# Performance work log

Measured on AMD Instinct MI355X. Metric: run time of the kernel, lower is better.

Reference implementation:

```python
import jax, jax.numpy as jnp
import numpy as np

B, S, H, NH = 2, 2048, 1024, 16
HD = H // NH  # head dim = 64


def setup_inputs() -> dict:
    key = jax.random.key(0)
    ks = jax.random.split(key, 11)
    s = 1.0 / np.sqrt(H)
    return {
        "q": jax.random.normal(ks[0], (B, S, H), jnp.float32),
        "k": jax.random.normal(ks[1], (B, S, H), jnp.float32),
        "v": jax.random.normal(ks[2], (B, S, H), jnp.float32),
        "Wq": jax.random.normal(ks[3], (H, H), jnp.float32) * s,
        "bq": jax.random.normal(ks[4], (H,), jnp.float32) * 0.02,
        "Wk": jax.random.normal(ks[5], (H, H), jnp.float32) * s,
        "bk": jax.random.normal(ks[6], (H,), jnp.float32) * 0.02,
        "Wv": jax.random.normal(ks[7], (H, H), jnp.float32) * s,
        "bv": jax.random.normal(ks[8], (H,), jnp.float32) * 0.02,
        "Wo": jax.random.normal(ks[9], (H, H), jnp.float32) * s,
        "bo": jax.random.normal(ks[10], (H,), jnp.float32) * 0.02,
    }


def reference(q, k, v, Wq, bq, Wk, bk, Wv, bv, Wo, bo):
    # QKV projections: [B,S,H]
    qp = q @ Wq + bq
    kp = k @ Wk + bk
    vp = v @ Wv + bv
    # split heads -> [B, NH, S, HD]
    def split(x):
        return x.reshape(B, S, NH, HD).transpose(0, 2, 1, 3)
    qh, kh, vh = split(qp), split(kp), split(vp)
    # scores [B, NH, S, S], scale by sqrt(head_dim)
    scores = jnp.einsum('bhqd,bhkd->bhqk', qh, kh) / jnp.sqrt(jnp.asarray(HD, qh.dtype))
    attn = jax.nn.softmax(scores, axis=-1)  # attention_dropout p=0.0 (eval)
    ctx = jnp.einsum('bhqk,bhkd->bhqd', attn, vh)
    # merge heads -> [B, S, H]
    ctx = ctx.transpose(0, 2, 1, 3).reshape(B, S, H)
    out = ctx @ Wo + bo  # dropout p=0.0 (eval)
    return out
```

## Files before the change

### kernel.cpp

```cpp
#include <hip/hip_runtime.h>

typedef unsigned short u16;
typedef __attribute__((ext_vector_type(8))) short bf16x8;
typedef __attribute__((ext_vector_type(4))) float f32x4;
typedef __attribute__((ext_vector_type(16))) float f32x16;
typedef __attribute__((ext_vector_type(4))) unsigned short u16x4;
typedef __attribute__((ext_vector_type(4))) unsigned int u32x4;

#define B_  2
#define S_  2048
#define H_  1024
#define NH_ 16
#define HD_ 64
#define MR_ (B_*S_)
#define K_  H_

__device__ __forceinline__ u16 f2bf(float f) {
  union { float f; unsigned u; } x; x.f = f;
  unsigned r = x.u + 0x7fffu + ((x.u >> 16) & 1u);
  return (u16)(r >> 16);
}

__device__ __forceinline__ unsigned cvtpk(float lo, float hi) {
  unsigned r;
  asm("v_cvt_pk_bf16_f32 %0, %1, %2" : "=v"(r) : "v"(lo), "v"(hi));
  return r;
}

__device__ __forceinline__ void gload16(const u16* g, u16* l) {
  __builtin_amdgcn_global_load_lds((const __attribute__((address_space(1))) void*)g,
                                   (__attribute__((address_space(3))) void*)l, 16, 0, 0);
}

__global__ __launch_bounds__(256) void cvt3(const float* __restrict__ q, const float* __restrict__ k,
                                            const float* __restrict__ v, u16* __restrict__ dst) {
  const float* src = blockIdx.z == 0 ? q : blockIdx.z == 1 ? k : v;
  u16* d = dst + (size_t)blockIdx.z * MR_ * H_;
  size_t i = ((size_t)blockIdx.x * 256 + threadIdx.x) * 4;
  float4 f = *(const float4*)(src + i);
  u16x4 o = { f2bf(f.x), f2bf(f.y), f2bf(f.z), f2bf(f.w) };
  *(u16x4*)(d + i) = o;
}

__global__ __launch_bounds__(256) void wtrans(const float* __restrict__ Wq, const float* __restrict__ Wk,
                                              const float* __restrict__ Wv, const float* __restrict__ Wo,
                                              u16* __restrict__ wt) {
  const int z = blockIdx.z;
  const float* W = z == 0 ? Wq : z == 1 ? Wk : z == 2 ? Wv : Wo;
  u16* Wt = wt + (size_t)z * H_ * K_;
  __shared__ float t[32][33];
  const int n0 = blockIdx.x * 32, k0 = blockIdx.y * 32;
  const int tx = threadIdx.x & 31, ty = threadIdx.x >> 5;
  #pragma unroll
  for (int i = 0; i < 4; i++) t[ty + 8*i][tx] = W[(size_t)(k0 + ty + 8*i) * H_ + n0 + tx];
  __syncthreads();
  #pragma unroll
  for (int i = 0; i < 4; i++) Wt[(size_t)(n0 + ty + 8*i) * K_ + k0 + tx] = f2bf(t[tx][ty + 8*i]);
}

template <int MODE>
__device__ __forceinline__ void gemm_body(const u16* __restrict__ A, const u16* __restrict__ Bt,
                                          const float* __restrict__ bias, float scale,
                                          u16* __restrict__ Obf, float* __restrict__ Of,
                                          int m_tile, int n_tile) {
  __shared__ u16 ldsA[128 * 64];
  __shared__ u16 ldsB[128 * 64];
  const int tid = threadIdx.x;
  const int lane = tid & 63, wave = tid >> 6;
  const int wm = wave >> 1, wn = wave & 1;
  const int m0 = m_tile * 128, n0 = n_tile * 128;

  f32x4 acc[4][4] = {};

  const int srow = tid >> 3;
  const int sslot = (tid & 7) ^ (srow & 7);
  const u16* ga = A + (size_t)(m0 + srow) * K_ + sslot * 8;
  const u16* gb = Bt + (size_t)(n0 + srow) * K_ + sslot * 8;
  u16* la = ldsA + tid * 8;
  u16* lb = ldsB + tid * 8;

  const int fr = lane & 15;
  const int kg = lane >> 4;

  for (int k0 = 0; k0 < K_; k0 += 64) {
    #pragma unroll
    for (int j = 0; j < 4; j++) gload16(ga + (size_t)(j * 32) * K_ + k0, la + j * 2048);
    #pragma unroll
    for (int j = 0; j < 4; j++) gload16(gb + (size_t)(j * 32) * K_ + k0, lb + j * 2048);
    __syncthreads();

    #pragma unroll
    for (int kk = 0; kk < 2; kk++) {
      const int ps = (((kk << 2) | kg) ^ (fr & 7)) * 8;
      bf16x8 a[4], b[4];
      #pragma unroll
      for (int mf = 0; mf < 4; mf++)
        a[mf] = *(const bf16x8*)&ldsA[(wm * 64 + mf * 16 + fr) * 64 + ps];
      #pragma unroll
      for (int nf = 0; nf < 4; nf++)
        b[nf] = *(const bf16x8*)&ldsB[(wn * 64 + nf * 16 + fr) * 64 + ps];
      #pragma unroll
      for (int mf = 0; mf < 4; mf++)
        #pragma unroll
        for (int nf = 0; nf < 4; nf++)
          acc[mf][nf] = __builtin_amdgcn_mfma_f32_16x16x32_bf16(a[mf], b[nf], acc[mf][nf], 0, 0, 0);
    }
    __syncthreads();
  }

  float bcol[4];
  #pragma unroll
  for (int nf = 0; nf < 4; nf++) bcol[nf] = bias[n0 + wn * 64 + nf * 16 + fr];

  if (MODE == 2) {
    #pragma unroll
    for (int mf = 0; mf < 4; mf++) {
      const int row0 = m0 + wm * 64 + mf * 16 + kg * 4;
      #pragma unroll
      for (int nf = 0; nf < 4; nf++) {
        const int col = n0 + wn * 64 + nf * 16 + fr;
        u16x4 o;
        #pragma unroll
        for (int r = 0; r < 4; r++) o[r] = f2bf(acc[mf][nf][r] + bcol[nf]);
        size_t idx = (((size_t)(col + ((row0 >> 11) << 10))) << 11) + (row0 & 2047);
        *(u16x4*)(Obf + idx) = o;
      }
    }
  } else {
    #pragma unroll
    for (int mf = 0; mf < 4; mf++)
      #pragma unroll
      for (int r = 0; r < 4; r++) {
        const int row = m0 + wm * 64 + mf * 16 + kg * 4 + r;
        #pragma unroll
        for (int nf = 0; nf < 4; nf++) {
          const int col = n0 + wn * 64 + nf * 16 + fr;
          float val = (acc[mf][nf][r] + bcol[nf]) * scale;
          if (MODE == 0) Obf[(size_t)row * H_ + col] = f2bf(val);
          else           Of [(size_t)row * H_ + col] = val;
        }
      }
  }
}

__global__ __launch_bounds__(256) void gemm_qkv(const u16* __restrict__ xb, const u16* __restrict__ wt,
                                                const float* __restrict__ b0, const float* __restrict__ b1,
                                                const float* __restrict__ b2,
                                                u16* __restrict__ QKo, u16* __restrict__ VTo) {
  const int z = blockIdx.z;
  const u16* A = xb + (size_t)z * MR_ * K_;
  const u16* Bt = wt + (size_t)z * H_ * K_;
  if (z == 2) {
    gemm_body<2>(A, Bt, b2, 1.0f, VTo, nullptr, blockIdx.y, blockIdx.x);
  } else {
    const float* bias = z == 0 ? b0 : b1;
    const float scale = z == 0 ? 0.18033688011112042f : 1.0f;
    gemm_body<0>(A, Bt, bias, scale, QKo + (size_t)z * MR_ * H_, nullptr, blockIdx.y, blockIdx.x);
  }
}

__global__ __launch_bounds__(256) void gemm_out(const u16* __restrict__ ctx, const u16* __restrict__ wot,
                                                const float* __restrict__ bo, float* __restrict__ out) {
  gemm_body<1>(ctx, wot, bo, 1.0f, nullptr, out, blockIdx.y, blockIdx.x);
}

__global__ __launch_bounds__(256) void attn(const u16* __restrict__ qp, const u16* __restrict__ kp,
                                            const u16* __restrict__ vt, u16* __restrict__ ctx) {
  __shared__ u16 Kl[2][64 * 64];
  __shared__ u16 Vl[2][64 * 64];
  const int bh = blockIdx.y;
  const int b = bh >> 4, h = bh & 15;
  const int q0 = blockIdx.x * 128;
  const int tid = threadIdx.x;
  const int w = tid >> 6, l = tid & 63;
  const int ql = l & 31, hi = l >> 5;

  const u16* Q   = qp + (size_t)b * S_ * H_ + h * HD_;
  const u16* Kb  = kp + (size_t)b * S_ * H_ + h * HD_;
  const u16* Vtb = vt + (size_t)bh * HD_ * S_;
  u16* O = ctx + (size_t)b * S_ * H_ + h * HD_;

  const int srow = tid >> 3;
  const int sslot = (tid & 7) ^ (srow & 7);

  const int qrow = q0 + w * 32 + ql;
  bf16x8 qf[4];
  #pragma unroll
  for (int ds = 0; ds < 4; ds++)
    qf[ds] = *(const bf16x8*)&Q[(size_t)qrow * H_ + ds * 16 + hi * 8];

  f32x16 oacc0 = {}, oacc1 = {};
  float m_run = -1e30f, l_run = 0.f;

  #pragma unroll
  for (int j = 0; j < 2; j++) {
    gload16(Kb + (size_t)(srow + 32 * j) * H_ + sslot * 8, &Kl[0][0] + j * 2048 + tid * 8);
    gload16(Vtb + (size_t)(srow + 32 * j) * S_ + sslot * 8, &Vl[0][0] + j * 2048 + tid * 8);
  }

  for (int it = 0; it < S_ / 64; ++it) {
    const int s0 = it * 64, cur = it & 1;
    __syncthreads();
    if (it + 1 < S_ / 64) {
      #pragma unroll
      for (int j = 0; j < 2; j++) {
        gload16(Kb + (size_t)(s0 + 64 + srow + 32 * j) * H_ + sslot * 8,
                &Kl[cur ^ 1][0] + j * 2048 + tid * 8);
        gload16(Vtb + (size_t)(srow + 32 * j) * S_ + s0 + 64 + sslot * 8,
                &Vl[cur ^ 1][0] + j * 2048 + tid * 8);
      }
    }
    f32x16 sc0 = {}, sc1 = {};
    __builtin_amdgcn_s_setprio(1);
    #pragma unroll
    for (int ds = 0; ds < 4; ds++) {
      const int sl = ((ds * 2 + hi) ^ (ql & 7)) << 3;
      bf16x8 k0 = *(const bf16x8*)&Kl[cur][ql * 64 + sl];
      bf16x8 k1 = *(const bf16x8*)&Kl[cur][(32 + ql) * 64 + sl];
      sc0 = __builtin_amdgcn_mfma_f32_32x32x16_bf16(k0, qf[ds], sc0, 0, 0, 0);
      sc1 = __builtin_amdgcn_mfma_f32_32x32x16_bf16(k1, qf[ds], sc1, 0, 0, 0);
    }
    __builtin_amdgcn_s_setprio(0);
    float t4[8];
    #pragma unroll
    for (int g = 0; g < 4; g++) {
      t4[g]     = fmaxf(fmaxf(sc0[4*g], sc0[4*g+1]), fmaxf(sc0[4*g+2], sc0[4*g+3]));
      t4[4 + g] = fmaxf(fmaxf(sc1[4*g], sc1[4*g+1]), fmaxf(sc1[4*g+2], sc1[4*g+3]));
    }
    float tmax = fmaxf(fmaxf(fmaxf(t4[0], t4[1]), fmaxf(t4[2], t4[3])),
                       fmaxf(fmaxf(t4[4], t4[5]), fmaxf(t4[6], t4[7])));
    tmax = fmaxf(tmax, __shfl_xor(tmax, 32, 64));
    if (!__all(tmax <= m_run + 8.0f)) {
      const float mn = fmaxf(m_run, tmax);
      const float sf = __builtin_amdgcn_exp2f(m_run - mn);
      m_run = mn;
      l_run *= sf;
      #pragma unroll
      for (int r = 0; r < 16; r++) {
        const float sfq = __shfl(sf, (r & 3) + 8 * (r >> 2) + 4 * hi, 64);
        oacc0[r] *= sfq;
        oacc1[r] *= sfq;
      }
    }
    float ps4[8];
    #pragma unroll
    for (int g = 0; g < 4; g++) {
      #pragma unroll
      for (int m = 0; m < 4; m++) {
        sc0[4*g+m] = __builtin_amdgcn_exp2f(sc0[4*g+m] - m_run);
        sc1[4*g+m] = __builtin_amdgcn_exp2f(sc1[4*g+m] - m_run);
      }
      ps4[g]     = (sc0[4*g] + sc0[4*g+1]) + (sc0[4*g+2] + sc0[4*g+3]);
      ps4[4 + g] = (sc1[4*g] + sc1[4*g+1]) + (sc1[4*g+2] + sc1[4*g+3]);
    }
    float psum = ((ps4[0] + ps4[1]) + (ps4[2] + ps4[3])) + ((ps4[4] + ps4[5]) + (ps4[6] + ps4[7]));
    psum += __shfl_xor(psum, 32, 64);
    l_run += psum;
    uint2 pk0[4], pk1[4];
    #pragma unroll
    for (int g = 0; g < 4; g++) {
      pk0[g].x = cvtpk(sc0[4*g], sc0[4*g+1]);  pk0[g].y = cvtpk(sc0[4*g+2], sc0[4*g+3]);
      pk1[g].x = cvtpk(sc1[4*g], sc1[4*g+1]);  pk1[g].y = cvtpk(sc1[4*g+2], sc1[4*g+3]);
    }
    __builtin_amdgcn_s_setprio(1);
    #pragma unroll
    for (int ks = 0; ks < 4; ks++) {
      const int gb = (ks & 1) * 2;
      const uint2 pa = (ks < 2) ? pk0[gb]     : pk1[gb];
      const uint2 pb = (ks < 2) ? pk0[gb + 1] : pk1[gb + 1];
      uint2 own, snd;
      own.x = hi ? pb.x : pa.x;  own.y = hi ? pb.y : pa.y;
      snd.x = hi ? pa.x : pb.x;  snd.y = hi ? pa.y : pb.y;
      uint2 rcv;
      rcv.x = __shfl_xor((int)snd.x, 32, 64);
      rcv.y = __shfl_xor((int)snd.y, 32, 64);
      u32x4 fu;
      fu.x = hi ? rcv.x : own.x;  fu.y = hi ? rcv.y : own.y;
      fu.z = hi ? own.x : rcv.x;  fu.w = hi ? own.y : rcv.y;
      const bf16x8 pfrag = __builtin_bit_cast(bf16x8, fu);
      #pragma unroll
      for (int dt = 0; dt < 2; dt++) {
        const int d = dt * 32 + ql;
        bf16x8 vf = *(const bf16x8*)&Vl[cur][d * 64 + (((ks * 2 + hi) ^ (d & 7)) << 3)];
        if (dt == 0) oacc0 = __builtin_amdgcn_mfma_f32_32x32x16_bf16(pfrag, vf, oacc0, 0, 0, 0);
        else         oacc1 = __builtin_amdgcn_mfma_f32_32x32x16_bf16(pfrag, vf, oacc1, 0, 0, 0);
      }
    }
    __builtin_amdgcn_s_setprio(0);
  }
  const float linv = 1.0f / l_run;
  #pragma unroll
  for (int r = 0; r < 16; r++) {
    const int qi = (r & 3) + 8 * (r >> 2) + 4 * hi;
    const float lq = __shfl(linv, qi, 64);
    const int row = q0 + w * 32 + qi;
    O[(size_t)row * H_ + ql]      = f2bf(oacc0[r] * lq);
    O[(size_t)row * H_ + 32 + ql] = f2bf(oacc1[r] * lq);
  }
}

extern "C" void kernel_launch(void* const* d_in, const int* in_sizes, int n_in,
                              void* d_out, int out_size, void* d_ws, size_t ws_size,
                              hipStream_t stream) {
  const float* q  = (const float*)d_in[0];
  const float* k  = (const float*)d_in[1];
  const float* v  = (const float*)d_in[2];
  const float* Wq = (const float*)d_in[3];
  const float* bq = (const float*)d_in[4];
  const float* Wk = (const float*)d_in[5];
  const float* bk = (const float*)d_in[6];
  const float* Wv = (const float*)d_in[7];
  const float* bv = (const float*)d_in[8];
  const float* Wo = (const float*)d_in[9];
  const float* bo = (const float*)d_in[10];
  float* out = (float*)d_out;

  char* ws = (char*)d_ws;
  const size_t MB = 1024 * 1024;
  u16* xb   = (u16*)(ws);
  u16* wt   = (u16*)(ws + 24 * MB);
  u16* qkp  = (u16*)(ws + 32 * MB);
  u16* vtp  = (u16*)(ws + 48 * MB);
  u16* ctx  = (u16*)(ws);

  cvt3  <<<dim3(4096, 1, 3), 256, 0, stream>>>(q, k, v, xb);
  wtrans<<<dim3(32, 32, 4),  256, 0, stream>>>(Wq, Wk, Wv, Wo, wt);
  gemm_qkv<<<dim3(8, 32, 3), 256, 0, stream>>>(xb, wt, bq, bk, bv, qkp, vtp);
  attn  <<<dim3(16, 32),     256, 0, stream>>>(qkp, qkp + (size_t)MR_ * H_, vtp, ctx);
  gemm_out<<<dim3(8, 32, 1), 256, 0, stream>>>(ctx, wt + (size_t)3 * H_ * K_, bo, out);
}
```

Before: 153.6 us.

## Split attention KV sequence across two wave groups and use permlane32 swap

The attention kernel now runs 512 threads per block. Two groups of four waves each process half of the key/value sequence (flash-decoding style split-K), and their partial max/sum and output accumulators are merged through shared memory at the end. This doubles wave-level parallelism for the 512-block grid, which is small relative to the CU count, and halves the serial KV loop length. The cost is extra LDS, more barriers, and a reduction epilogue. The cross-half shuffle used to build the P fragment is also replaced with the v_permlane32_swap instruction to cut the shuffle and select overhead.

```diff
diff --git a/kernel.cpp b/kernel.cpp
--- a/kernel.cpp
+++ b/kernel.cpp
@@ -25,6 +25,10 @@
   unsigned r;
   asm("v_cvt_pk_bf16_f32 %0, %1, %2" : "=v"(r) : "v"(lo), "v"(hi));
   return r;
+}
+
+__device__ __forceinline__ void plswap(unsigned &a, unsigned &b) {
+  asm("v_permlane32_swap_b32 %0, %1" : "+v"(a), "+v"(b));
 }
 
 __device__ __forceinline__ void gload16(const u16* g, u16* l) {
@@ -164,15 +168,19 @@
   gemm_body<1>(ctx, wot, bo, 1.0f, nullptr, out, blockIdx.y, blockIdx.x);
 }
 
-__global__ __launch_bounds__(256) void attn(const u16* __restrict__ qp, const u16* __restrict__ kp,
+__global__ __launch_bounds__(512) void attn(const u16* __restrict__ qp, const u16* __restrict__ kp,
                                             const u16* __restrict__ vt, u16* __restrict__ ctx) {
-  __shared__ u16 Kl[2][64 * 64];
-  __shared__ u16 Vl[2][64 * 64];
+  __shared__ u16 Kl[2][2][64 * 64];
+  __shared__ u16 Vl[2][2][64 * 64];
+  __shared__ float mlbuf[2][4][32][2];
   const int bh = blockIdx.y;
   const int b = bh >> 4, h = bh & 15;
   const int q0 = blockIdx.x * 128;
   const int tid = threadIdx.x;
-  const int w = tid >> 6, l = tid & 63;
+  const int g0 = tid >> 8;
+  const int gt = tid & 255;
+  const int w = (tid >> 6) & 3;
+  const int l = tid & 63;
   const int ql = l & 31, hi = l >> 5;
 
   const u16* Q   = qp + (size_t)b * S_ * H_ + h * HD_;
@@ -180,8 +188,9 @@
   const u16* Vtb = vt + (size_t)bh * HD_ * S_;
   u16* O = ctx + (size_t)b * S_ * H_ + h * HD_;
 
-  const int srow = tid >> 3;
-  const int sslot = (tid & 7) ^ (srow & 7);
+  const int srow = gt >> 3;
+  const int sslot = (gt & 7) ^ (srow & 7);
+  const int sbase = g0 << 10;
 
   const int qrow = q0 + w * 32 + ql;
   bf16x8 qf[4];
@@ -194,20 +203,22 @@
 
   #pragma unroll
   for (int j = 0; j < 2; j++) {
-    gload16(Kb + (size_t)(srow + 32 * j) * H_ + sslot * 8, &Kl[0][0] + j * 2048 + tid * 8);
-    gload16(Vtb + (size_t)(srow + 32 * j) * S_ + sslot * 8, &Vl[0][0] + j * 2048 + tid * 8);
-  }
-
-  for (int it = 0; it < S_ / 64; ++it) {
-    const int s0 = it * 64, cur = it & 1;
+    gload16(Kb + (size_t)(sbase + srow + 32 * j) * H_ + sslot * 8,
+            &Kl[g0][0][0] + j * 2048 + gt * 8);
+    gload16(Vtb + (size_t)(srow + 32 * j) * S_ + sbase + sslot * 8,
+            &Vl[g0][0][0] + j * 2048 + gt * 8);
+  }
+
+  for (int it = 0; it < 16; ++it) {
+    const int s0 = sbase + it * 64, cur = it & 1;
     __syncthreads();
-    if (it + 1 < S_ / 64) {
+    if (it + 1 < 16) {
       #pragma unroll
       for (int j = 0; j < 2; j++) {
         gload16(Kb + (size_t)(s0 + 64 + srow + 32 * j) * H_ + sslot * 8,
-                &Kl[cur ^ 1][0] + j * 2048 + tid * 8);
+                &Kl[g0][cur ^ 1][0] + j * 2048 + gt * 8);
         gload16(Vtb + (size_t)(srow + 32 * j) * S_ + s0 + 64 + sslot * 8,
-                &Vl[cur ^ 1][0] + j * 2048 + tid * 8);
+                &Vl[g0][cur ^ 1][0] + j * 2048 + gt * 8);
       }
     }
     f32x16 sc0 = {}, sc1 = {};
@@ -215,8 +226,8 @@
     #pragma unroll
     for (int ds = 0; ds < 4; ds++) {
       const int sl = ((ds * 2 + hi) ^ (ql & 7)) << 3;
-      bf16x8 k0 = *(const bf16x8*)&Kl[cur][ql * 64 + sl];
-      bf16x8 k1 = *(const bf16x8*)&Kl[cur][(32 + ql) * 64 + sl];
+      bf16x8 k0 = *(const bf16x8*)&Kl[g0][cur][ql * 64 + sl];
+      bf16x8 k1 = *(const bf16x8*)&Kl[g0][cur][(32 + ql) * 64 + sl];
       sc0 = __builtin_amdgcn_mfma_f32_32x32x16_bf16(k0, qf[ds], sc0, 0, 0, 0);
       sc1 = __builtin_amdgcn_mfma_f32_32x32x16_bf16(k1, qf[ds], sc1, 0, 0, 0);
     }
@@ -265,37 +276,58 @@
     __builtin_amdgcn_s_setprio(1);
     #pragma unroll
     for (int ks = 0; ks < 4; ks++) {
-      const int gb = (ks & 1) * 2;
-      const uint2 pa = (ks < 2) ? pk0[gb]     : pk1[gb];
-      const uint2 pb = (ks < 2) ? pk0[gb + 1] : pk1[gb + 1];
-      uint2 own, snd;
-      own.x = hi ? pb.x : pa.x;  own.y = hi ? pb.y : pa.y;
-      snd.x = hi ? pa.x : pb.x;  snd.y = hi ? pa.y : pb.y;
-      uint2 rcv;
-      rcv.x = __shfl_xor((int)snd.x, 32, 64);
-      rcv.y = __shfl_xor((int)snd.y, 32, 64);
-      u32x4 fu;
-      fu.x = hi ? rcv.x : own.x;  fu.y = hi ? rcv.y : own.y;
-      fu.z = hi ? own.x : rcv.x;  fu.w = hi ? own.y : rcv.y;
+      const int ga = (ks & 1) * 2;
+      unsigned x0, y0, x1, y1;
+      if (ks < 2) { x0 = pk0[ga].x; y0 = pk0[ga].y; x1 = pk0[ga+1].x; y1 = pk0[ga+1].y; }
+      else        { x0 = pk1[ga].x; y0 = pk1[ga].y; x1 = pk1[ga+1].x; y1 = pk1[ga+1].y; }
+      plswap(x0, x1);
+      plswap(y0, y1);
+      u32x4 fu = { x0, y0, x1, y1 };
       const bf16x8 pfrag = __builtin_bit_cast(bf16x8, fu);
       #pragma unroll
       for (int dt = 0; dt < 2; dt++) {
         const int d = dt * 32 + ql;
-        bf16x8 vf = *(const bf16x8*)&Vl[cur][d * 64 + (((ks * 2 + hi) ^ (d & 7)) << 3)];
+        bf16x8 vf = *(const bf16x8*)&Vl[g0][cur][d * 64 + (((ks * 2 + hi) ^ (d & 7)) << 3)];
         if (dt == 0) oacc0 = __builtin_amdgcn_mfma_f32_32x32x16_bf16(pfrag, vf, oacc0, 0, 0, 0);
         else         oacc1 = __builtin_amdgcn_mfma_f32_32x32x16_bf16(pfrag, vf, oacc1, 0, 0, 0);
       }
     }
     __builtin_amdgcn_s_setprio(0);
   }
-  const float linv = 1.0f / l_run;
+
+  if (l < 32) { mlbuf[g0][w][ql][0] = m_run; mlbuf[g0][w][ql][1] = l_run; }
+  __syncthreads();
+  const float m_o = mlbuf[g0 ^ 1][w][ql][0];
+  const float l_o = mlbuf[g0 ^ 1][w][ql][1];
+  const float m_tot = fmaxf(m_run, m_o);
+  const float a_s = __builtin_amdgcn_exp2f(m_run - m_tot);
+  const float rinv = 1.0f / (l_run * a_s + l_o * __builtin_amdgcn_exp2f(m_o - m_tot));
+  float ar[16], rr[16];
   #pragma unroll
   for (int r = 0; r < 16; r++) {
     const int qi = (r & 3) + 8 * (r >> 2) + 4 * hi;
-    const float lq = __shfl(linv, qi, 64);
-    const int row = q0 + w * 32 + qi;
-    O[(size_t)row * H_ + ql]      = f2bf(oacc0[r] * lq);
-    O[(size_t)row * H_ + 32 + ql] = f2bf(oacc1[r] * lq);
+    ar[r] = __shfl(a_s, qi, 64);
+    rr[r] = __shfl(rinv, qi, 64);
+  }
+
+  float* cb = (float*)(&Kl[0][0][0]);
+  float* cw = cb + w * 2048 + l;
+  if (g0 == 1) {
+    #pragma unroll
+    for (int r = 0; r < 16; r++) {
+      cw[r * 64]        = oacc0[r] * ar[r];
+      cw[(16 + r) * 64] = oacc1[r] * ar[r];
+    }
+  }
+  __syncthreads();
+  if (g0 == 0) {
+    #pragma unroll
+    for (int r = 0; r < 16; r++) {
+      const int qi = (r & 3) + 8 * (r >> 2) + 4 * hi;
+      const int row = q0 + w * 32 + qi;
+      O[(size_t)row * H_ + ql]      = f2bf((oacc0[r] * ar[r] + cw[r * 64]) * rr[r]);
+      O[(size_t)row * H_ + 32 + ql] = f2bf((oacc1[r] * ar[r] + cw[(16 + r) * 64]) * rr[r]);
+    }
   }
 }
 
@@ -326,6 +358,6 @@
   cvt3  <<<dim3(4096, 1, 3), 256, 0, stream>>>(q, k, v, xb);
   wtrans<<<dim3(32, 32, 4),  256, 0, stream>>>(Wq, Wk, Wv, Wo, wt);
   gemm_qkv<<<dim3(8, 32, 3), 256, 0, stream>>>(xb, wt, bq, bk, bv, qkp, vtp);
-  attn  <<<dim3(16, 32),     256, 0, stream>>>(qkp, qkp + (size_t)MR_ * H_, vtp, ctx);
+  attn  <<<dim3(16, 32),     512, 0, stream>>>(qkp, qkp + (size_t)MR_ * H_, vtp, ctx);
   gemm_out<<<dim3(8, 32, 1), 256, 0, stream>>>(ctx, wt + (size_t)3 * H_ * K_, bo, out);
 }
```

New measurement: 154.0 us. Within noise of the previous version (+0.3%).
